# Performance work log

Measured on AMD Instinct MI355X. Metric: run time of the kernel, lower is better.

Reference implementation:

```python
import jax, jax.numpy as jnp
import numpy as np

B, M, E, D = 8, 8192, 2048, 64  # batch, nodes, hyperedges, feature dim (in_feats == out_feats required by the einsum)


def setup_inputs() -> dict:
    key = jax.random.key(0)
    k1, k2, k3, k4, k5 = jax.random.split(key, 5)
    inc_mat = (jax.random.uniform(k1, (B, M, E)) < 0.02).astype(jnp.float32)
    edge_features = jax.random.normal(k2, (B, E, D), dtype=jnp.float32)
    prev_node_features = jax.random.normal(k3, (B, M, D), dtype=jnp.float32)
    scale = 1.0 / np.sqrt(D)
    Wa = jax.random.normal(k4, (D, D), dtype=jnp.float32) * scale  # attention Linear weight (out, in)
    Wp = jax.random.normal(k5, (D, D), dtype=jnp.float32) * scale  # projection Linear weight (out, in)
    alpha = jnp.float32(0.5)
    return {"inc_mat": inc_mat, "edge_features": edge_features,
            "prev_node_features": prev_node_features, "Wa": Wa, "Wp": Wp, "alpha": alpha}


def reference(inc_mat, edge_features, prev_node_features, Wa, Wp, alpha):
    # edge_attention_scores = attention(edge_features): (b, e, d)
    edge_scores = jnp.einsum('bed,od->beo', edge_features, Wa)
    # node_attention_scores = bmm(inc_mat, edge_scores): (b, m, d)
    node_scores = jnp.einsum('bme,bed->bmd', inc_mat, edge_scores)
    # softmax over the node dim (dim=1 in torch)
    attn = jax.nn.softmax(node_scores, axis=1)
    # einsum('bed,bme->bmed') followed by einsum('bmed,bmd->bmd') reduces exactly to
    # (inc_mat @ edge_features) * attn — attention weights are independent of e.
    agg = jnp.einsum('bme,bed->bmd', inc_mat, edge_features)
    weighted = agg * attn
    node_features = jnp.einsum('bmd,od->bmo', weighted, Wp)
    return alpha * prev_node_features + (1.0 - alpha) * node_features
```

## Files before the change

### kernel.cpp

```cpp
#include <hip/hip_runtime.h>

#define NB 8
#define NM 8192
#define NE 2048
#define ND 64

typedef unsigned long long u64;
typedef unsigned short u16;

constexpr int CAP     = 128;
constexpr int K1_ROWS = 32;
constexpr int K1_NBLK = NM / K1_ROWS;
constexpr int K4_ROWS = 64;
constexpr int K4_NBLK = NM / K4_ROWS;
constexpr int NROWS   = NB * NM;

__global__ __launch_bounds__(256) void k0_pack(const float* __restrict__ inc,
                                               u16* __restrict__ lists,
                                               int* __restrict__ counts) {
    const int lane = threadIdx.x & 63;
    const int gw   = (int)((blockIdx.x * 256u + threadIdx.x) >> 6);
    const int nw   = (int)((gridDim.x * 256u) >> 6);
    for (int row = gw; row < NROWS; row += nw) {
        const float4* rp = reinterpret_cast<const float4*>(inc + (size_t)row * NE);
        float4 v[8];
        #pragma unroll
        for (int c = 0; c < 8; ++c) v[c] = rp[c * 64 + lane];

        u16* lst = lists + (size_t)row * CAP;
        int base = 0;
        #pragma unroll
        for (int c = 0; c < 8; ++c) {
            const float x[4] = { v[c].x, v[c].y, v[c].z, v[c].w };
            #pragma unroll
            for (int q = 0; q < 4; ++q) {
                u64 m = __ballot(x[q] != 0.f);
                int below = __builtin_amdgcn_mbcnt_hi((unsigned)(m >> 32),
                            __builtin_amdgcn_mbcnt_lo((unsigned)m, 0));
                int pos = base + below;
                if (x[q] != 0.f && pos < CAP)
                    lst[pos] = (u16)(c * 256 + lane * 4 + q);
                base += __popcll(m);
            }
        }
        if (lane == 0) counts[row] = base < CAP ? base : CAP;
    }
}

__global__ __launch_bounds__(256) void k1_gather(
    const u16* __restrict__ lists,
    const int* __restrict__ counts,
    const float* __restrict__ ef,
    const float* __restrict__ Wa,
    float* __restrict__ agg,
    float* __restrict__ pmax,
    float* __restrict__ psum)
{
    __shared__ float WaT[ND * ND];
    __shared__ float rowbuf[4][ND];
    __shared__ float smax[4][ND];
    __shared__ float ssum[4][ND];

    const int tid  = threadIdx.x;
    const int lane = tid & 63;
    const int wave = tid >> 6;
    const int b    = blockIdx.x & 7;
    const int blk  = blockIdx.x >> 3;

    for (int i = tid; i < ND * ND; i += 256) {
        int o = i >> 6, d = i & 63;
        WaT[d * ND + o] = Wa[i];
    }
    __syncthreads();

    const float* efb = ef + (size_t)b * (NE * ND);

    float runmax = -INFINITY, runsum = 0.f;

    for (int r = 0; r < K1_ROWS / 4; ++r) {
        const int m   = blk * K1_ROWS + r * 4 + wave;
        const int row = b * NM + m;
        const int cnt = counts[row];
        const unsigned pw = reinterpret_cast<const unsigned*>(
                                lists + (size_t)row * CAP)[lane];

        float a0 = 0.f, a1 = 0.f, a2 = 0.f, a3 = 0.f,
              a4 = 0.f, a5 = 0.f, a6 = 0.f, a7 = 0.f;
        int i = 0;
        for (; i + 8 <= cnt; i += 8) {
            const int h = i >> 1;
            unsigned w0 = __shfl(pw, h),     w1 = __shfl(pw, h + 1);
            unsigned w2 = __shfl(pw, h + 2), w3 = __shfl(pw, h + 3);
            a0 += efb[(size_t)(w0 & 0xffffu) * ND + lane];
            a1 += efb[(size_t)(w0 >> 16)     * ND + lane];
            a2 += efb[(size_t)(w1 & 0xffffu) * ND + lane];
            a3 += efb[(size_t)(w1 >> 16)     * ND + lane];
            a4 += efb[(size_t)(w2 & 0xffffu) * ND + lane];
            a5 += efb[(size_t)(w2 >> 16)     * ND + lane];
            a6 += efb[(size_t)(w3 & 0xffffu) * ND + lane];
            a7 += efb[(size_t)(w3 >> 16)     * ND + lane];
        }
        for (; i < cnt; ++i) {
            unsigned w = __shfl(pw, i >> 1);
            unsigned idx = (i & 1) ? (w >> 16) : (w & 0xffffu);
            a0 += efb[(size_t)idx * ND + lane];
        }
        const float acc = ((a0 + a1) + (a2 + a3)) + ((a4 + a5) + (a6 + a7));

        agg[((size_t)b * NM + m) * ND + lane] = acc;

        rowbuf[wave][lane] = acc;
        float s = 0.f;
        #pragma unroll
        for (int d = 0; d < ND; ++d)
            s = fmaf(rowbuf[wave][d], WaT[d * ND + lane], s);

        float nm = fmaxf(runmax, s);
        runsum = runsum * __expf(runmax - nm) + __expf(s - nm);
        runmax = nm;
    }

    smax[wave][lane] = runmax;
    ssum[wave][lane] = runsum;
    __syncthreads();
    if (wave == 0) {
        float gm = smax[0][lane], gs = ssum[0][lane];
        for (int w = 1; w < 4; ++w) {
            float wm = smax[w][lane], ws = ssum[w][lane];
            float nm = fmaxf(gm, wm);
            gs = gs * __expf(gm - nm) + ws * __expf(wm - nm);
            gm = nm;
        }
        pmax[((size_t)b * K1_NBLK + blk) * ND + lane] = gm;
        psum[((size_t)b * K1_NBLK + blk) * ND + lane] = gs;
    }
}

__global__ __launch_bounds__(256) void k3_combine(
    const float* __restrict__ pmax, const float* __restrict__ psum,
    float* __restrict__ gmaxv, float* __restrict__ gsumv)
{
    __shared__ float smax[4][ND], ssum[4][ND];
    const int b = blockIdx.x, d = threadIdx.x & 63, c = threadIdx.x >> 6;
    float gm = -INFINITY, gs = 0.f;
    for (int i = c; i < K1_NBLK; i += 4) {
        float wm = pmax[((size_t)b * K1_NBLK + i) * ND + d];
        float ws = psum[((size_t)b * K1_NBLK + i) * ND + d];
        float nm = fmaxf(gm, wm);
        gs = gs * __expf(gm - nm) + ws * __expf(wm - nm);
        gm = nm;
    }
    smax[c][d] = gm; ssum[c][d] = gs;
    __syncthreads();
    if (c == 0) {
        for (int w = 1; w < 4; ++w) {
            float wm = smax[w][d], ws = ssum[w][d];
            float nm = fmaxf(gm, wm);
            gs = gs * __expf(gm - nm) + ws * __expf(wm - nm);
            gm = nm;
        }
        gmaxv[b * ND + d] = gm;
        gsumv[b * ND + d] = gs;
    }
}

__global__ __launch_bounds__(256) void k4_final(
    const float* __restrict__ agg, const float* __restrict__ Wa,
    const float* __restrict__ Wp, const float* __restrict__ prev,
    const float* __restrict__ gmaxv, const float* __restrict__ gsumv,
    const float* __restrict__ alpha_p, float* __restrict__ out)
{
    __shared__ float WaT[ND * ND], WpT[ND * ND];
    __shared__ float rowA[4][ND], rowW[4][ND];
    const int tid = threadIdx.x, lane = tid & 63, wave = tid >> 6;
    const int b = blockIdx.x / K4_NBLK, blk = blockIdx.x % K4_NBLK;

    for (int i = tid; i < ND * ND; i += 256) {
        int o = i >> 6, d = i & 63;
        WaT[d * ND + o] = Wa[i];
        WpT[d * ND + o] = Wp[i];
    }
    __syncthreads();

    const float alpha = alpha_p[0];
    const float gmax = gmaxv[b * ND + lane];
    const float inv  = 1.0f / gsumv[b * ND + lane];

    for (int r = 0; r < K4_ROWS / 4; ++r) {
        const int m = blk * K4_ROWS + r * 4 + wave;
        const size_t ro = ((size_t)b * NM + m) * ND;
        const float a = agg[ro + lane];

        rowA[wave][lane] = a;
        float s = 0.f;
        #pragma unroll
        for (int d = 0; d < ND; ++d)
            s = fmaf(rowA[wave][d], WaT[d * ND + lane], s);

        const float attn = __expf(s - gmax) * inv;
        rowW[wave][lane] = a * attn;
        float nf = 0.f;
        #pragma unroll
        for (int d = 0; d < ND; ++d)
            nf = fmaf(rowW[wave][d], WpT[d * ND + lane], nf);

        out[ro + lane] = alpha * prev[ro + lane] + (1.f - alpha) * nf;
    }
}

extern "C" void kernel_launch(void* const* d_in, const int* in_sizes, int n_in,
                              void* d_out, int out_size, void* d_ws, size_t ws_size,
                              hipStream_t stream) {
    const float* inc     = (const float*)d_in[0];
    const float* ef      = (const float*)d_in[1];
    const float* prev    = (const float*)d_in[2];
    const float* Wa      = (const float*)d_in[3];
    const float* Wp      = (const float*)d_in[4];
    const float* alpha_p = (const float*)d_in[5];
    float* out = (float*)d_out;

    float* agg   = (float*)d_ws;
    float* pmax  = agg   + (size_t)NB * NM * ND;
    float* psum  = pmax  + (size_t)NB * K1_NBLK * ND;
    float* gmaxv = psum  + (size_t)NB * K1_NBLK * ND;
    float* gsumv = gmaxv + NB * ND;
    int*   counts = (int*)(gsumv + NB * ND);
    u16*   lists  = (u16*)(counts + NROWS);

    k0_pack  <<<2048, 256, 0, stream>>>(inc, lists, counts);
    k1_gather<<<2048, 256, 0, stream>>>(lists, counts, ef, Wa, agg, pmax, psum);
    k3_combine<<<NB, 256, 0, stream>>>(pmax, psum, gmaxv, gsumv);
    k4_final <<<NB * K4_NBLK, 256, 0, stream>>>(agg, Wa, Wp, prev, gmaxv, gsumv, alpha_p, out);
}
```

Baseline: 261.8 us.

## Keep weight rows in registers with lane broadcasts and cache attention scores

Each lane now holds one weight row (Wa or Wp) in 64 registers, and the row vector is broadcast across the wave with readlane, replacing the shared-memory transposed weight tiles and row buffers. The gather kernel also writes the computed attention scores to a new workspace buffer, so the final kernel reads them instead of recomputing the Wa matvec. This removes the LDS staging and barriers and halves the matvec work in the final kernel. In exchange it adds a 16 MB score write and read, and raises register pressure, which may lower occupancy.

```diff
diff --git a/kernel.cpp b/kernel.cpp
--- a/kernel.cpp
+++ b/kernel.cpp
@@ -14,6 +14,10 @@
 constexpr int K4_ROWS = 64;
 constexpr int K4_NBLK = NM / K4_ROWS;
 constexpr int NROWS   = NB * NM;
+
+__device__ __forceinline__ float bcast(float v, int d) {
+    return __uint_as_float(__builtin_amdgcn_readlane(__float_as_uint(v), d));
+}
 
 __global__ __launch_bounds__(256) void k0_pack(const float* __restrict__ inc,
                                                u16* __restrict__ lists,
@@ -53,11 +57,10 @@
     const float* __restrict__ ef,
     const float* __restrict__ Wa,
     float* __restrict__ agg,
+    float* __restrict__ score,
     float* __restrict__ pmax,
     float* __restrict__ psum)
 {
-    __shared__ float WaT[ND * ND];
-    __shared__ float rowbuf[4][ND];
     __shared__ float smax[4][ND];
     __shared__ float ssum[4][ND];
 
@@ -67,11 +70,12 @@
     const int b    = blockIdx.x & 7;
     const int blk  = blockIdx.x >> 3;
 
-    for (int i = tid; i < ND * ND; i += 256) {
-        int o = i >> 6, d = i & 63;
-        WaT[d * ND + o] = Wa[i];
-    }
-    __syncthreads();
+    float wa[ND];
+    #pragma unroll
+    for (int k = 0; k < ND / 4; ++k) {
+        float4 t = reinterpret_cast<const float4*>(Wa + (size_t)lane * ND)[k];
+        wa[4 * k] = t.x; wa[4 * k + 1] = t.y; wa[4 * k + 2] = t.z; wa[4 * k + 3] = t.w;
+    }
 
     const float* efb = ef + (size_t)b * (NE * ND);
 
@@ -107,13 +111,14 @@
         }
         const float acc = ((a0 + a1) + (a2 + a3)) + ((a4 + a5) + (a6 + a7));
 
-        agg[((size_t)b * NM + m) * ND + lane] = acc;
-
-        rowbuf[wave][lane] = acc;
+        const size_t ro = ((size_t)b * NM + m) * ND;
+        agg[ro + lane] = acc;
+
         float s = 0.f;
         #pragma unroll
         for (int d = 0; d < ND; ++d)
-            s = fmaf(rowbuf[wave][d], WaT[d * ND + lane], s);
+            s = fmaf(bcast(acc, d), wa[d], s);
+        score[ro + lane] = s;
 
         float nm = fmaxf(runmax, s);
         runsum = runsum * __expf(runmax - nm) + __expf(s - nm);
@@ -165,22 +170,20 @@
 }
 
 __global__ __launch_bounds__(256) void k4_final(
-    const float* __restrict__ agg, const float* __restrict__ Wa,
+    const float* __restrict__ agg, const float* __restrict__ score,
     const float* __restrict__ Wp, const float* __restrict__ prev,
     const float* __restrict__ gmaxv, const float* __restrict__ gsumv,
     const float* __restrict__ alpha_p, float* __restrict__ out)
 {
-    __shared__ float WaT[ND * ND], WpT[ND * ND];
-    __shared__ float rowA[4][ND], rowW[4][ND];
     const int tid = threadIdx.x, lane = tid & 63, wave = tid >> 6;
     const int b = blockIdx.x / K4_NBLK, blk = blockIdx.x % K4_NBLK;
 
-    for (int i = tid; i < ND * ND; i += 256) {
-        int o = i >> 6, d = i & 63;
-        WaT[d * ND + o] = Wa[i];
-        WpT[d * ND + o] = Wp[i];
-    }
-    __syncthreads();
+    float wp[ND];
+    #pragma unroll
+    for (int k = 0; k < ND / 4; ++k) {
+        float4 t = reinterpret_cast<const float4*>(Wp + (size_t)lane * ND)[k];
+        wp[4 * k] = t.x; wp[4 * k + 1] = t.y; wp[4 * k + 2] = t.z; wp[4 * k + 3] = t.w;
+    }
 
     const float alpha = alpha_p[0];
     const float gmax = gmaxv[b * ND + lane];
@@ -190,19 +193,15 @@
         const int m = blk * K4_ROWS + r * 4 + wave;
         const size_t ro = ((size_t)b * NM + m) * ND;
         const float a = agg[ro + lane];
-
-        rowA[wave][lane] = a;
-        float s = 0.f;
+        const float s = score[ro + lane];
+
+        const float attn = __expf(s - gmax) * inv;
+        const float w = a * attn;
+
+        float nf = 0.f;
         #pragma unroll
         for (int d = 0; d < ND; ++d)
-            s = fmaf(rowA[wave][d], WaT[d * ND + lane], s);
-
-        const float attn = __expf(s - gmax) * inv;
-        rowW[wave][lane] = a * attn;
-        float nf = 0.f;
-        #pragma unroll
-        for (int d = 0; d < ND; ++d)
-            nf = fmaf(rowW[wave][d], WpT[d * ND + lane], nf);
+            nf = fmaf(bcast(w, d), wp[d], nf);
 
         out[ro + lane] = alpha * prev[ro + lane] + (1.f - alpha) * nf;
     }
@@ -220,7 +219,8 @@
     float* out = (float*)d_out;
 
     float* agg   = (float*)d_ws;
-    float* pmax  = agg   + (size_t)NB * NM * ND;
+    float* scorev= agg   + (size_t)NB * NM * ND;
+    float* pmax  = scorev+ (size_t)NB * NM * ND;
     float* psum  = pmax  + (size_t)NB * K1_NBLK * ND;
     float* gmaxv = psum  + (size_t)NB * K1_NBLK * ND;
     float* gsumv = gmaxv + NB * ND;
@@ -228,7 +228,7 @@
     u16*   lists  = (u16*)(counts + NROWS);
 
     k0_pack  <<<2048, 256, 0, stream>>>(inc, lists, counts);
-    k1_gather<<<2048, 256, 0, stream>>>(lists, counts, ef, Wa, agg, pmax, psum);
+    k1_gather<<<2048, 256, 0, stream>>>(lists, counts, ef, Wa, agg, scorev, pmax, psum);
     k3_combine<<<NB, 256, 0, stream>>>(pmax, psum, gmaxv, gsumv);
-    k4_final <<<NB * K4_NBLK, 256, 0, stream>>>(agg, Wa, Wp, prev, gmaxv, gsumv, alpha_p, out);
-}
+    k4_final <<<NB * K4_NBLK, 256, 0, stream>>>(agg, scorev, Wp, prev, gmaxv, gsumv, alpha_p, out);
+}
```

After: 253.3 us. 1.03x faster.
